# Kernel optimization log

Hardware: AMD Instinct MI355X
Metric: run time of the kernel (lower is better)

The kernel has to match this reference:

```python
import jax, jax.numpy as jnp
import numpy as np

B, S, IN_DIM = 8, 1024, 512
EMBED_DIM, NUM_HEADS = 512, 8
HEAD_DIM = EMBED_DIM // NUM_HEADS
LN_EPS = 1e-5


def setup_inputs() -> dict:
    key = jax.random.key(0)
    k1, k2, k3 = jax.random.split(key, 3)
    x = jax.random.normal(k1, (B, S, IN_DIM), dtype=jnp.float32)
    # xavier_uniform for qkv_proj.weight [3*embed, in] and o_proj.weight [embed, embed]
    lim_qkv = float(np.sqrt(6.0 / (3 * EMBED_DIM + IN_DIM)))
    w_qkv = jax.random.uniform(k2, (3 * EMBED_DIM, IN_DIM), dtype=jnp.float32,
                               minval=-lim_qkv, maxval=lim_qkv)
    lim_o = float(np.sqrt(6.0 / (EMBED_DIM + EMBED_DIM)))
    w_o = jax.random.uniform(k3, (EMBED_DIM, EMBED_DIM), dtype=jnp.float32,
                             minval=-lim_o, maxval=lim_o)
    return {"x": x, "w_qkv": w_qkv, "w_o": w_o}


def reference(x, w_qkv, w_o):
    b, s, _ = x.shape
    # fused QKV projection: [b, s, 3*embed]
    qkv = jnp.einsum('bsi,ei->bse', x, w_qkv)
    # [b, h, s, 3*head_dim]
    qkv = qkv.reshape(b, s, NUM_HEADS, 3 * HEAD_DIM).transpose(0, 2, 1, 3)
    q, k, v = jnp.split(qkv, 3, axis=-1)
    scale = 1.0 / np.sqrt(HEAD_DIM)
    logits = jnp.einsum('bhqd,bhkd->bhqk', q, k) * scale  # [b, h, s, s]
    attn = jax.nn.softmax(logits, axis=-1)
    vals = jnp.einsum('bhqk,bhkd->bhqd', attn, v)
    vals = vals.transpose(0, 2, 1, 3).reshape(b, s, EMBED_DIM)
    o = jnp.einsum('bse,fe->bsf', vals, w_o)
    # LayerNorm over [seq, embed] jointly (fresh nn.LayerNorm([N, D]): weight=1, bias=0)
    mu = jnp.mean(o, axis=(-2, -1), keepdims=True)
    var = jnp.var(o, axis=(-2, -1), keepdims=True)
    o = (o - mu) / jnp.sqrt(var + LN_EPS)
    return o
```

## Files before the change

### kernel.cpp

```cpp
#include <hip/hip_runtime.h>
#include <hip/hip_bf16.h>
#include <math.h>

#define BB 8
#define SS 1024
#define INDIM 512
#define ED 512
#define NH 8
#define HD 64

typedef __attribute__((ext_vector_type(8))) short short8;
typedef __attribute__((ext_vector_type(4))) float f32x4;
typedef __attribute__((ext_vector_type(16))) float f32x16;
typedef unsigned short u16;

typedef __attribute__((address_space(1))) const void gv_t;
typedef __attribute__((address_space(3))) void lv_t;

static __device__ __forceinline__ u16 f2bf(float f) {
  union { float f; unsigned u; } v; v.f = f;
  unsigned r = v.u + 0x7fffu + ((v.u >> 16) & 1u);
  return (u16)(r >> 16);
}

static __device__ __forceinline__ unsigned cvt_pk_bf16(float a, float b) {
  unsigned r;
  asm("v_cvt_pk_bf16_f32 %0, %1, %2" : "=v"(r) : "v"(a), "v"(b));
  return r;
}
static __device__ __forceinline__ float fast_exp2(float x) {
  float r; asm("v_exp_f32 %0, %1" : "=v"(r) : "v"(x)); return r;
}

__global__ void cvt_all(const float* __restrict__ x, const float* __restrict__ wq,
                        const float* __restrict__ wo, u16* __restrict__ xb,
                        u16* __restrict__ wqb, u16* __restrict__ wob) {
  const int n1 = 1048576;
  const int n2 = n1 + 196608;
  const int n3 = n2 + 65536;
  int i = blockIdx.x * blockDim.x + threadIdx.x;
  int stride = gridDim.x * blockDim.x;
  for (; i < n3; i += stride) {
    const float4* src; ushort4* dst; int j;
    if (i < n1)      { src = (const float4*)x;  dst = (ushort4*)xb;  j = i; }
    else if (i < n2) { src = (const float4*)wq; dst = (ushort4*)wqb; j = i - n1; }
    else             { src = (const float4*)wo; dst = (ushort4*)wob; j = i - n2; }
    float4 v = src[j];
    ushort4 o;
    o.x = f2bf(v.x); o.y = f2bf(v.y); o.z = f2bf(v.z); o.w = f2bf(v.w);
    dst[j] = o;
  }
}

template<int EPI>
__global__ __launch_bounds__(256, 2)
void gemm_nt(const u16* __restrict__ A, const u16* __restrict__ Bm, int K,
             float* __restrict__ outF,
             u16* __restrict__ qws, u16* __restrict__ kws, u16* __restrict__ vtws,
             float* __restrict__ partials, unsigned* __restrict__ counter)
{
  __shared__ u16 As[128][64];
  __shared__ u16 Bs[128][64];
  const int tid = threadIdx.x;
  const int lane = tid & 63;
  const int wv = tid >> 6;
  const int wr = wv >> 1, wc = wv & 1;
  const int bm = blockIdx.x, bn = blockIdx.y;
  const int l15 = lane & 15, lg = lane >> 4;
  const int srow8 = lane >> 3;
  const int sc8 = lane & 7;

  f32x4 acc[4][4];
  #pragma unroll
  for (int i = 0; i < 4; i++)
    #pragma unroll
    for (int j = 0; j < 4; j++) acc[i][j] = (f32x4){0.f, 0.f, 0.f, 0.f};

  for (int kk = 0; kk < K; kk += 64) {
    #pragma unroll
    for (int i = 0; i < 4; i++) {
      int r0 = (i * 4 + wv) * 8;
      int r = r0 + srow8;
      int cs = sc8 ^ (r & 7);
      const u16* ga = A + (size_t)(bm * 128 + r) * K + kk + cs * 8;
      __builtin_amdgcn_global_load_lds((gv_t*)ga, (lv_t*)&As[r0][0], 16, 0, 0);
      const u16* gb = Bm + (size_t)(bn * 128 + r) * K + kk + cs * 8;
      __builtin_amdgcn_global_load_lds((gv_t*)gb, (lv_t*)&Bs[r0][0], 16, 0, 0);
    }
    __syncthreads();
    #pragma unroll
    for (int kc = 0; kc < 2; kc++) {
      short8 af[4], bf[4];
      #pragma unroll
      for (int mi = 0; mi < 4; mi++) {
        int ra = wr * 64 + mi * 16 + l15;
        af[mi] = *(const short8*)&As[ra][((kc * 4 + lg) ^ (ra & 7)) * 8];
      }
      #pragma unroll
      for (int ni = 0; ni < 4; ni++) {
        int rb = wc * 64 + ni * 16 + l15;
        bf[ni] = *(const short8*)&Bs[rb][((kc * 4 + lg) ^ (rb & 7)) * 8];
      }
      #pragma unroll
      for (int mi = 0; mi < 4; mi++)
        #pragma unroll
        for (int ni = 0; ni < 4; ni++)
          acc[mi][ni] = __builtin_amdgcn_mfma_f32_16x16x32_bf16(af[mi], bf[ni], acc[mi][ni], 0, 0, 0);
    }
    __syncthreads();
  }

  if (EPI == 0) {
    #pragma unroll
    for (int mi = 0; mi < 4; mi++) {
      int rowg = bm * 128 + wr * 64 + mi * 16 + lg * 4;
      #pragma unroll
      for (int ni = 0; ni < 4; ni++) {
        int colg = bn * 128 + wc * 64 + ni * 16 + l15;
        #pragma unroll
        for (int r = 0; r < 4; r++) {
          int rg = rowg + r;
          float v = acc[mi][ni][r];
          int b = rg >> 10, s = rg & 1023;
          int h = colg / 192, c = colg - h * 192;
          int bh = b * 8 + h;
          if (c < 64)
            qws[((size_t)(bh * 1024 + s)) * 64 + c] = f2bf(v * 0.18033688f);
          else if (c < 128)
            kws[((size_t)(bh * 1024 + s)) * 64 + (c - 64)] = f2bf(v);
          else
            vtws[((size_t)(bh * 64 + (c - 128))) * 1024 + s] = f2bf(v);
        }
      }
    }
  } else {
    float s1 = 0.f, s2 = 0.f;
    #pragma unroll
    for (int mi = 0; mi < 4; mi++)
      #pragma unroll
      for (int ni = 0; ni < 4; ni++)
        #pragma unroll
        for (int r = 0; r < 4; r++) {
          float v = acc[mi][ni][r];
          s1 += v; s2 += v * v;
        }
    #pragma unroll
    for (int off = 1; off < 64; off <<= 1) {
      s1 += __shfl_xor(s1, off);
      s2 += __shfl_xor(s2, off);
    }
    __shared__ float r1[4], r2[4];
    __shared__ float musr[2];
    if (lane == 0) { r1[wv] = s1; r2[wv] = s2; }
    __syncthreads();
    if (tid == 0) {
      float t1 = r1[0] + r1[1] + r1[2] + r1[3];
      float t2 = r2[0] + r2[1] + r2[2] + r2[3];
      int pid = (bm * 4 + bn) * 2;
      atomicExch(&partials[pid], t1);
      atomicExch(&partials[pid + 1], t2);
      __threadfence();
      atomicAdd(counter, 1u);
      while (atomicAdd(counter, 0u) < 256u) {}
    }
    __syncthreads();
    if (wv == 0) {
      float a = 0.f, c = 0.f;
      if (lane < 32) {
        int base = ((bm >> 3) * 32 + lane) * 2;
        a = atomicAdd(&partials[base], 0.0f);
        c = atomicAdd(&partials[base + 1], 0.0f);
      }
      #pragma unroll
      for (int off = 1; off < 64; off <<= 1) {
        a += __shfl_xor(a, off);
        c += __shfl_xor(c, off);
      }
      if (lane == 0) {
        float mu = a / 524288.f;
        float var = c / 524288.f - mu * mu;
        musr[0] = mu;
        musr[1] = rsqrtf(var + 1e-5f);
      }
    }
    __syncthreads();
    float mu = musr[0], rs = musr[1];
    #pragma unroll
    for (int mi = 0; mi < 4; mi++) {
      int rowg = bm * 128 + wr * 64 + mi * 16 + lg * 4;
      #pragma unroll
      for (int ni = 0; ni < 4; ni++) {
        int colg = bn * 128 + wc * 64 + ni * 16 + l15;
        #pragma unroll
        for (int r = 0; r < 4; r++)
          outF[(size_t)(rowg + r) * 512 + colg] = (acc[mi][ni][r] - mu) * rs;
      }
    }
  }
}

__global__ __launch_bounds__(256, 2)
void attn_kernel(const u16* __restrict__ qws, const u16* __restrict__ kws,
                 const u16* __restrict__ vtws, u16* __restrict__ vals)
{
  __shared__ __align__(16) u16 Ksm[2][64][72];
  __shared__ __align__(16) u16 Vsm[2][64][72];
  const int tid = threadIdx.x;
  const int lane = tid & 63;
  const int wq = tid >> 6;
  const int l31 = lane & 31;
  const int hi = lane >> 5;
  const int logical = (blockIdx.x & 7) * 64 + (blockIdx.x >> 3);
  const int bh = logical >> 3;
  const int q0 = (logical & 7) * 128;

  short8 qf[4];
  {
    const u16* qp = qws + ((size_t)bh * 1024 + q0 + wq * 32 + l31) * 64 + 8 * hi;
    #pragma unroll
    for (int j = 0; j < 4; j++) qf[j] = *(const short8*)(qp + 16 * j);
  }

  const int srow = tid >> 3;
  const int sc8 = (tid & 7) * 8;
  uint4 kreg[2], vreg[2];
  {
    kreg[0] = *(const uint4*)(kws + ((size_t)bh * 1024 + srow) * 64 + sc8);
    kreg[1] = *(const uint4*)(kws + ((size_t)bh * 1024 + srow + 32) * 64 + sc8);
    vreg[0] = *(const uint4*)(vtws + ((size_t)(bh * 64 + srow)) * 1024 + sc8);
    vreg[1] = *(const uint4*)(vtws + ((size_t)(bh * 64 + srow + 32)) * 1024 + sc8);
    *(uint4*)&Ksm[0][srow][sc8] = kreg[0];
    *(uint4*)&Ksm[0][srow + 32][sc8] = kreg[1];
    *(uint4*)&Vsm[0][srow][sc8] = vreg[0];
    *(uint4*)&Vsm[0][srow + 32][sc8] = vreg[1];
  }
  __syncthreads();

  f32x16 o[2];
  #pragma unroll
  for (int r = 0; r < 16; r++) { o[0][r] = 0.f; o[1][r] = 0.f; }
  float m = -1e30f, l = 0.f;

  for (int t = 0; t < 16; t++) {
    const int cur = t & 1;
    if (t < 15) {
      int kv = (t + 1) * 64;
      kreg[0] = *(const uint4*)(kws + ((size_t)bh * 1024 + kv + srow) * 64 + sc8);
      kreg[1] = *(const uint4*)(kws + ((size_t)bh * 1024 + kv + srow + 32) * 64 + sc8);
      vreg[0] = *(const uint4*)(vtws + ((size_t)(bh * 64 + srow)) * 1024 + kv + sc8);
      vreg[1] = *(const uint4*)(vtws + ((size_t)(bh * 64 + srow + 32)) * 1024 + kv + sc8);
    }

    f32x16 stv[2];
    __builtin_amdgcn_s_setprio(1);
    #pragma unroll
    for (int s2 = 0; s2 < 2; s2++) {
      f32x16 c;
      #pragma unroll
      for (int r = 0; r < 16; r++) c[r] = 0.f;
      #pragma unroll
      for (int j = 0; j < 4; j++) {
        short8 kf = *(const short8*)&Ksm[cur][s2 * 32 + l31][16 * j + 8 * hi];
        c = __builtin_amdgcn_mfma_f32_32x32x16_bf16(kf, qf[j], c, 0, 0, 0);
      }
      stv[s2] = c;
    }
    __builtin_amdgcn_s_setprio(0);

    float mx[16];
    #pragma unroll
    for (int r = 0; r < 16; r++) mx[r] = fmaxf(stv[0][r], stv[1][r]);
    #pragma unroll
    for (int w = 8; w >= 1; w >>= 1)
      #pragma unroll
      for (int r = 0; r < w; r++) mx[r] = fmaxf(mx[r], mx[r + w]);
    float pm = fmaxf(mx[0], __shfl_xor(mx[0], 32));

    if (!__all(pm - m <= 10.0f)) {
      float mn = fmaxf(m, pm);
      float al = fast_exp2(m - mn);
      m = mn; l *= al;
      #pragma unroll
      for (int reg = 0; reg < 16; reg++) {
        int qrow = (reg & 3) + 8 * (reg >> 2) + 4 * hi;
        float alo = __shfl(al, qrow);
        o[0][reg] *= alo; o[1][reg] *= alo;
      }
    }

    unsigned pk[16];
    float ps[16];
    #pragma unroll
    for (int s2 = 0; s2 < 2; s2++)
      #pragma unroll
      for (int j = 0; j < 8; j++) {
        float p0 = fast_exp2(stv[s2][2 * j] - m);
        float p1 = fast_exp2(stv[s2][2 * j + 1] - m);
        ps[s2 * 8 + j] = p0 + p1;
        pk[s2 * 8 + j] = cvt_pk_bf16(p0, p1);
      }
    #pragma unroll
    for (int w = 8; w >= 1; w >>= 1)
      #pragma unroll
      for (int r = 0; r < w; r++) ps[r] += ps[r + w];
    l += ps[0] + __shfl_xor(ps[0], 32);

    short8 pa[4];
    #pragma unroll
    for (int cc = 0; cc < 4; cc++) {
      int base = (cc >> 1) * 8 + (cc & 1) * 4;
      unsigned a0 = pk[base + 0], a2 = pk[base + 2];
      unsigned a1 = pk[base + 1], a3 = pk[base + 3];
      asm volatile("v_permlane32_swap_b32 %0, %1" : "+v"(a0), "+v"(a2));
      asm volatile("v_permlane32_swap_b32 %0, %1" : "+v"(a1), "+v"(a3));
      union { unsigned u[4]; short8 s8; } uu;
      uu.u[0] = a0; uu.u[1] = a1; uu.u[2] = a2; uu.u[3] = a3;
      pa[cc] = uu.s8;
    }

    __builtin_amdgcn_s_setprio(1);
    #pragma unroll
    for (int dh = 0; dh < 2; dh++)
      #pragma unroll
      for (int cc = 0; cc < 4; cc++) {
        short8 vf = *(const short8*)&Vsm[cur][dh * 32 + l31][16 * cc + 8 * hi];
        o[dh] = __builtin_amdgcn_mfma_f32_32x32x16_bf16(pa[cc], vf, o[dh], 0, 0, 0);
      }
    __builtin_amdgcn_s_setprio(0);

    if (t < 15) {
      *(uint4*)&Ksm[cur ^ 1][srow][sc8] = kreg[0];
      *(uint4*)&Ksm[cur ^ 1][srow + 32][sc8] = kreg[1];
      *(uint4*)&Vsm[cur ^ 1][srow][sc8] = vreg[0];
      *(uint4*)&Vsm[cur ^ 1][srow + 32][sc8] = vreg[1];
    }
    __syncthreads();
  }

  const int b = bh >> 3, h = bh & 7;
  #pragma unroll
  for (int reg = 0; reg < 16; reg++) {
    int qrow = (reg & 3) + 8 * (reg >> 2) + 4 * hi;
    float linv = 1.0f / __shfl(l, qrow);
    size_t grow = (size_t)(b * 1024 + q0 + wq * 32 + qrow) * 512 + h * 64;
    vals[grow + l31]      = f2bf(o[0][reg] * linv);
    vals[grow + 32 + l31] = f2bf(o[1][reg] * linv);
  }
}

extern "C" void kernel_launch(void* const* d_in, const int* in_sizes, int n_in,
                              void* d_out, int out_size, void* d_ws, size_t ws_size,
                              hipStream_t stream) {
  const float* x = (const float*)d_in[0];
  const float* wqkv = (const float*)d_in[1];
  const float* wo = (const float*)d_in[2];
  float* out = (float*)d_out;
  char* ws = (char*)d_ws;

  u16* xb        = (u16*)(ws + 0);
  u16* wqb       = (u16*)(ws + 8388608);
  u16* wob       = (u16*)(ws + 9961472);
  u16* qws       = (u16*)(ws + 10485760);
  u16* kws       = (u16*)(ws + 18874368);
  u16* vtws      = (u16*)(ws + 27262976);
  u16* vals      = (u16*)(ws + 35651584);
  unsigned* ctr  = (unsigned*)(ws + 44040192);
  float* parts   = (float*)(ws + 44040256);

  hipMemsetAsync(ctr, 0, 4, stream);

  cvt_all<<<1280, 256, 0, stream>>>(x, wqkv, wo, xb, wqb, wob);

  dim3 g1(64, 12);
  gemm_nt<0><<<g1, 256, 0, stream>>>(xb, wqb, 512, nullptr, qws, kws, vtws, nullptr, nullptr);

  attn_kernel<<<512, 256, 0, stream>>>(qws, kws, vtws, vals);

  dim3 g2(64, 4);
  gemm_nt<1><<<g2, 256, 0, stream>>>(vals, wob, 512, out, nullptr, nullptr, nullptr, parts, ctr);
}
```

Before: 93.96 us.

## Replace grid spin barrier with separate LN kernel; read K/V directly from global

The output GEMM now writes unnormalized results plus per-block partial sums, and a new ln_norm2 kernel applies the joint LayerNorm. This replaces the in-kernel atomic counter spin barrier and drops the memset. Separately, the attention kernel no longer stages K/V through double-buffered LDS with syncthreads; each lane loads its MFMA fragments straight from global memory, relying on cache reuse. The trade is an extra read-write pass over the output, plus uncoalesced, repeated global loads of K/V across waves.

```diff
diff --git a/kernel.cpp b/kernel.cpp
--- a/kernel.cpp
+++ b/kernel.cpp
@@ -57,7 +57,7 @@
 void gemm_nt(const u16* __restrict__ A, const u16* __restrict__ Bm, int K,
              float* __restrict__ outF,
              u16* __restrict__ qws, u16* __restrict__ kws, u16* __restrict__ vtws,
-             float* __restrict__ partials, unsigned* __restrict__ counter)
+             float2* __restrict__ partials)
 {
   __shared__ u16 As[128][64];
   __shared__ u16 Bs[128][64];
@@ -136,65 +136,31 @@
   } else {
     float s1 = 0.f, s2 = 0.f;
     #pragma unroll
-    for (int mi = 0; mi < 4; mi++)
-      #pragma unroll
-      for (int ni = 0; ni < 4; ni++)
+    for (int mi = 0; mi < 4; mi++) {
+      int rowg = bm * 128 + wr * 64 + mi * 16 + lg * 4;
+      #pragma unroll
+      for (int ni = 0; ni < 4; ni++) {
+        int colg = bn * 128 + wc * 64 + ni * 16 + l15;
         #pragma unroll
         for (int r = 0; r < 4; r++) {
           float v = acc[mi][ni][r];
           s1 += v; s2 += v * v;
+          outF[(size_t)(rowg + r) * 512 + colg] = v;
         }
+      }
+    }
     #pragma unroll
     for (int off = 1; off < 64; off <<= 1) {
       s1 += __shfl_xor(s1, off);
       s2 += __shfl_xor(s2, off);
     }
     __shared__ float r1[4], r2[4];
-    __shared__ float musr[2];
     if (lane == 0) { r1[wv] = s1; r2[wv] = s2; }
     __syncthreads();
     if (tid == 0) {
       float t1 = r1[0] + r1[1] + r1[2] + r1[3];
       float t2 = r2[0] + r2[1] + r2[2] + r2[3];
-      int pid = (bm * 4 + bn) * 2;
-      atomicExch(&partials[pid], t1);
-      atomicExch(&partials[pid + 1], t2);
-      __threadfence();
-      atomicAdd(counter, 1u);
-      while (atomicAdd(counter, 0u) < 256u) {}
-    }
-    __syncthreads();
-    if (wv == 0) {
-      float a = 0.f, c = 0.f;
-      if (lane < 32) {
-        int base = ((bm >> 3) * 32 + lane) * 2;
-        a = atomicAdd(&partials[base], 0.0f);
-        c = atomicAdd(&partials[base + 1], 0.0f);
-      }
-      #pragma unroll
-      for (int off = 1; off < 64; off <<= 1) {
-        a += __shfl_xor(a, off);
-        c += __shfl_xor(c, off);
-      }
-      if (lane == 0) {
-        float mu = a / 524288.f;
-        float var = c / 524288.f - mu * mu;
-        musr[0] = mu;
-        musr[1] = rsqrtf(var + 1e-5f);
-      }
-    }
-    __syncthreads();
-    float mu = musr[0], rs = musr[1];
-    #pragma unroll
-    for (int mi = 0; mi < 4; mi++) {
-      int rowg = bm * 128 + wr * 64 + mi * 16 + lg * 4;
-      #pragma unroll
-      for (int ni = 0; ni < 4; ni++) {
-        int colg = bn * 128 + wc * 64 + ni * 16 + l15;
-        #pragma unroll
-        for (int r = 0; r < 4; r++)
-          outF[(size_t)(rowg + r) * 512 + colg] = (acc[mi][ni][r] - mu) * rs;
-      }
+      partials[bm * 4 + bn] = make_float2(t1, t2);
     }
   }
 }
@@ -203,8 +169,6 @@
 void attn_kernel(const u16* __restrict__ qws, const u16* __restrict__ kws,
                  const u16* __restrict__ vtws, u16* __restrict__ vals)
 {
-  __shared__ __align__(16) u16 Ksm[2][64][72];
-  __shared__ __align__(16) u16 Vsm[2][64][72];
   const int tid = threadIdx.x;
   const int lane = tid & 63;
   const int wq = tid >> 6;
@@ -220,21 +184,8 @@
     #pragma unroll
     for (int j = 0; j < 4; j++) qf[j] = *(const short8*)(qp + 16 * j);
   }
-
-  const int srow = tid >> 3;
-  const int sc8 = (tid & 7) * 8;
-  uint4 kreg[2], vreg[2];
-  {
-    kreg[0] = *(const uint4*)(kws + ((size_t)bh * 1024 + srow) * 64 + sc8);
-    kreg[1] = *(const uint4*)(kws + ((size_t)bh * 1024 + srow + 32) * 64 + sc8);
-    vreg[0] = *(const uint4*)(vtws + ((size_t)(bh * 64 + srow)) * 1024 + sc8);
-    vreg[1] = *(const uint4*)(vtws + ((size_t)(bh * 64 + srow + 32)) * 1024 + sc8);
-    *(uint4*)&Ksm[0][srow][sc8] = kreg[0];
-    *(uint4*)&Ksm[0][srow + 32][sc8] = kreg[1];
-    *(uint4*)&Vsm[0][srow][sc8] = vreg[0];
-    *(uint4*)&Vsm[0][srow + 32][sc8] = vreg[1];
-  }
-  __syncthreads();
+  const u16* kbase = kws + (size_t)bh * 1024 * 64 + (size_t)l31 * 64 + 8 * hi;
+  const u16* vbase = vtws + ((size_t)(bh * 64 + l31)) * 1024 + 8 * hi;
 
   f32x16 o[2];
   #pragma unroll
@@ -242,14 +193,7 @@
   float m = -1e30f, l = 0.f;
 
   for (int t = 0; t < 16; t++) {
-    const int cur = t & 1;
-    if (t < 15) {
-      int kv = (t + 1) * 64;
-      kreg[0] = *(const uint4*)(kws + ((size_t)bh * 1024 + kv + srow) * 64 + sc8);
-      kreg[1] = *(const uint4*)(kws + ((size_t)bh * 1024 + kv + srow + 32) * 64 + sc8);
-      vreg[0] = *(const uint4*)(vtws + ((size_t)(bh * 64 + srow)) * 1024 + kv + sc8);
-      vreg[1] = *(const uint4*)(vtws + ((size_t)(bh * 64 + srow + 32)) * 1024 + kv + sc8);
-    }
+    const int kv = t * 64;
 
     f32x16 stv[2];
     __builtin_amdgcn_s_setprio(1);
@@ -260,7 +204,7 @@
       for (int r = 0; r < 16; r++) c[r] = 0.f;
       #pragma unroll
       for (int j = 0; j < 4; j++) {
-        short8 kf = *(const short8*)&Ksm[cur][s2 * 32 + l31][16 * j + 8 * hi];
+        short8 kf = *(const short8*)(kbase + (size_t)(kv + s2 * 32) * 64 + 16 * j);
         c = __builtin_amdgcn_mfma_f32_32x32x16_bf16(kf, qf[j], c, 0, 0, 0);
       }
       stv[s2] = c;
@@ -323,18 +267,10 @@
     for (int dh = 0; dh < 2; dh++)
       #pragma unroll
       for (int cc = 0; cc < 4; cc++) {
-        short8 vf = *(const short8*)&Vsm[cur][dh * 32 + l31][16 * cc + 8 * hi];
+        short8 vf = *(const short8*)(vbase + (size_t)dh * 32 * 1024 + kv + 16 * cc);
         o[dh] = __builtin_amdgcn_mfma_f32_32x32x16_bf16(pa[cc], vf, o[dh], 0, 0, 0);
       }
     __builtin_amdgcn_s_setprio(0);
-
-    if (t < 15) {
-      *(uint4*)&Ksm[cur ^ 1][srow][sc8] = kreg[0];
-      *(uint4*)&Ksm[cur ^ 1][srow + 32][sc8] = kreg[1];
-      *(uint4*)&Vsm[cur ^ 1][srow][sc8] = vreg[0];
-      *(uint4*)&Vsm[cur ^ 1][srow + 32][sc8] = vreg[1];
-    }
-    __syncthreads();
   }
 
   const int b = bh >> 3, h = bh & 7;
@@ -345,6 +281,33 @@
     size_t grow = (size_t)(b * 1024 + q0 + wq * 32 + qrow) * 512 + h * 64;
     vals[grow + l31]      = f2bf(o[0][reg] * linv);
     vals[grow + 32 + l31] = f2bf(o[1][reg] * linv);
+  }
+}
+
+__global__ void ln_norm2(float* __restrict__ o, const float2* __restrict__ partials) {
+  const int blk = blockIdx.x;
+  const int b = blk >> 8;
+  const int lane = threadIdx.x & 63;
+  float s1 = 0.f, s2 = 0.f;
+  if (lane < 32) {
+    float2 p = partials[b * 32 + lane];
+    s1 = p.x; s2 = p.y;
+  }
+  #pragma unroll
+  for (int off = 1; off < 64; off <<= 1) {
+    s1 += __shfl_xor(s1, off);
+    s2 += __shfl_xor(s2, off);
+  }
+  float mu = s1 / 524288.f;
+  float rs = rsqrtf(s2 / 524288.f - mu * mu + 1e-5f);
+  const int base = blk * 512;
+  #pragma unroll
+  for (int k = 0; k < 2; k++) {
+    int i = base + threadIdx.x + k * 256;
+    float4 v = ((const float4*)o)[i];
+    v.x = (v.x - mu) * rs; v.y = (v.y - mu) * rs;
+    v.z = (v.z - mu) * rs; v.w = (v.w - mu) * rs;
+    ((float4*)o)[i] = v;
   }
 }
 
@@ -364,18 +327,17 @@
   u16* kws       = (u16*)(ws + 18874368);
   u16* vtws      = (u16*)(ws + 27262976);
   u16* vals      = (u16*)(ws + 35651584);
-  unsigned* ctr  = (unsigned*)(ws + 44040192);
-  float* parts   = (float*)(ws + 44040256);
-
-  hipMemsetAsync(ctr, 0, 4, stream);
+  float2* parts  = (float2*)(ws + 44040192);
 
   cvt_all<<<1280, 256, 0, stream>>>(x, wqkv, wo, xb, wqb, wob);
 
   dim3 g1(64, 12);
-  gemm_nt<0><<<g1, 256, 0, stream>>>(xb, wqb, 512, nullptr, qws, kws, vtws, nullptr, nullptr);
+  gemm_nt<0><<<g1, 256, 0, stream>>>(xb, wqb, 512, nullptr, qws, kws, vtws, nullptr);
 
   attn_kernel<<<512, 256, 0, stream>>>(qws, kws, vtws, vals);
 
   dim3 g2(64, 4);
-  gemm_nt<1><<<g2, 256, 0, stream>>>(vals, wob, 512, out, nullptr, nullptr, nullptr, parts, ctr);
-}
+  gemm_nt<1><<<g2, 256, 0, stream>>>(vals, wob, 512, out, nullptr, nullptr, nullptr, parts);
+
+  ln_norm2<<<2048, 256, 0, stream>>>(out, parts);
+}
```

Result: slower. 115.9 us (+23.3%).
